# Kernel tuning notes

Measured on AMD Instinct MI355X. Metric: run time of the kernel, lower is better.

The kernel has to match this reference:

```python
import jax, jax.numpy as jnp
import numpy as np
import math

INPUT_SIZE = 2048
OUTPUT_SIZE = 10000
EPS = 1e-8


def _hadamard_cropped(rows, cols):
    # Sylvester Hadamard: H[i, j] = (-1) ** popcount(i & j), built only on the
    i = np.arange(rows, dtype=np.int64)[:, None]
    j = np.arange(cols, dtype=np.int64)[None, :]
    a = i & j
    nbits = max(rows, cols).bit_length()
    parity = np.zeros((rows, cols), dtype=np.int64)
    for k in range(nbits):
        parity += (a >> k) & 1
    return (1 - 2 * (parity & 1)).astype(np.float32)


def setup_inputs() -> dict:
    key = jax.random.key(0)
    kx, kb = jax.random.split(key)
    init_scale = 1.0 / math.sqrt(OUTPUT_SIZE)
    x = jax.random.normal(kx, (16384, INPUT_SIZE), dtype=jnp.float32)
    proj = jnp.asarray(_hadamard_cropped(OUTPUT_SIZE, INPUT_SIZE))
    scale = jnp.full((1,), init_scale, dtype=jnp.float32)
    bias = jax.random.uniform(kb, (OUTPUT_SIZE,), dtype=jnp.float32,
                              minval=-init_scale, maxval=init_scale)
    return {"x": x, "proj": proj, "scale": scale, "bias": bias}


def reference(x, proj, scale, bias):
    # L2-normalize along last dim (norm + eps, matching torch semantics)
    xn = x / (jnp.linalg.norm(x, axis=-1, keepdims=True) + EPS)
    # linear with cropped Hadamard matrix: [B, in] @ [out, in]^T -> [B, out]
    out = -scale * jnp.einsum('bi,oi->bo', xn, proj)
    return out + bias[None, :]
```

## Files before the change

kernel.cpp:

```cpp
#include <hip/hip_runtime.h>
#include <math.h>


typedef float f32x4 __attribute__((ext_vector_type(4)));

constexpr int N_IN  = 2048;
constexpr int N_OUT = 10000;
constexpr int ROWS_PER_BLOCK = 4;

__global__ __launch_bounds__(256, 4) void fwht_proj_kernel(
    const float* __restrict__ x,
    const float* __restrict__ scale,
    const float* __restrict__ bias,
    float* __restrict__ out)
{
    const int wave = threadIdx.x >> 6;
    const int lane = threadIdx.x & 63;
    const int row  = (blockIdx.x << 2) + wave;

    const float* __restrict__ xrow = x + (size_t)row * N_IN;

    f32x4 v[8];
    float ss = 0.0f;
#pragma unroll
    for (int j = 0; j < 8; ++j) {
        v[j] = *reinterpret_cast<const f32x4*>(xrow + (j << 8) + (lane << 2));
        ss = fmaf(v[j].x, v[j].x, ss);
        ss = fmaf(v[j].y, v[j].y, ss);
        ss = fmaf(v[j].z, v[j].z, ss);
        ss = fmaf(v[j].w, v[j].w, ss);
    }
#pragma unroll
    for (int m = 1; m < 64; m <<= 1)
        ss += __shfl_xor(ss, m, 64);
    const float inv = 1.0f / (sqrtf(ss) + 1e-8f);

#pragma unroll
    for (int j = 0; j < 8; ++j) {
        const f32x4 a = v[j];
        f32x4 t;
        t.x = a.x + a.y;  t.y = a.x - a.y;
        t.z = a.z + a.w;  t.w = a.z - a.w;
        f32x4 u;
        u.x = t.x + t.z;  u.y = t.y + t.w;
        u.z = t.x - t.z;  u.w = t.y - t.w;
        v[j] = u;
    }
#pragma unroll
    for (int m = 1; m <= 32; m <<= 1) {
        const bool lo = (lane & m) == 0;
#pragma unroll
        for (int j = 0; j < 8; ++j) {
            f32x4 o;
            o.x = __shfl_xor(v[j].x, m, 64);
            o.y = __shfl_xor(v[j].y, m, 64);
            o.z = __shfl_xor(v[j].z, m, 64);
            o.w = __shfl_xor(v[j].w, m, 64);
            v[j] = lo ? (v[j] + o) : (o - v[j]);
        }
    }
#pragma unroll
    for (int jm = 1; jm <= 4; jm <<= 1) {
#pragma unroll
        for (int j = 0; j < 8; ++j) {
            if ((j & jm) == 0) {
                const f32x4 a = v[j], b = v[j ^ jm];
                v[j]      = a + b;
                v[j ^ jm] = a - b;
            }
        }
    }

    const float s = -scale[0] * inv;
    float* __restrict__ orow = out + (size_t)row * N_OUT;

#pragma unroll
    for (int w = 0; w < 4; ++w) {
#pragma unroll 4
        for (int j = 0; j < 8; ++j) {
            const int o = (w << 11) + (j << 8) + (lane << 2);
            const f32x4 b = *reinterpret_cast<const f32x4*>(bias + o);
            f32x4 r;
            r.x = fmaf(s, v[j].x, b.x);
            r.y = fmaf(s, v[j].y, b.y);
            r.z = fmaf(s, v[j].z, b.z);
            r.w = fmaf(s, v[j].w, b.w);
            *reinterpret_cast<f32x4*>(orow + o) = r;
        }
    }
#pragma unroll 4
    for (int j = 0; j < 7; ++j) {
        const int o = 8192 + (j << 8) + (lane << 2);
        const f32x4 b = *reinterpret_cast<const f32x4*>(bias + o);
        f32x4 r;
        r.x = fmaf(s, v[j].x, b.x);
        r.y = fmaf(s, v[j].y, b.y);
        r.z = fmaf(s, v[j].z, b.z);
        r.w = fmaf(s, v[j].w, b.w);
        *reinterpret_cast<f32x4*>(orow + o) = r;
    }
    if (lane < 4) {
        const int o = 9984 + (lane << 2);
        const f32x4 b = *reinterpret_cast<const f32x4*>(bias + o);
        f32x4 r;
        r.x = fmaf(s, v[7].x, b.x);
        r.y = fmaf(s, v[7].y, b.y);
        r.z = fmaf(s, v[7].z, b.z);
        r.w = fmaf(s, v[7].w, b.w);
        *reinterpret_cast<f32x4*>(orow + o) = r;
    }
}

extern "C" void kernel_launch(void* const* d_in, const int* in_sizes, int n_in,
                              void* d_out, int out_size, void* d_ws, size_t ws_size,
                              hipStream_t stream) {
    const float* x     = (const float*)d_in[0];
    const float* scale = (const float*)d_in[2];
    const float* bias  = (const float*)d_in[3];
    float* out = (float*)d_out;

    const int rows = in_sizes[0] / N_IN;
    dim3 grid(rows / ROWS_PER_BLOCK), block(256);
    hipLaunchKernelGGL(fwht_proj_kernel, grid, block, 0, stream,
                       x, scale, bias, out);
}
```

Measured before the change: 177.4 us.

## Replace cross-lane shuffle butterflies with swizzled LDS transposes in FWHT

Six rounds of 32 shuffle_xor butterflies across lanes are replaced by an in-register butterfly, a transpose through per-wave shared memory with an XOR swizzle, one shuffle stage, and more in-register butterflies. A second swizzled LDS pass puts the results back in output order before the bias-add stores. The aim is to cut the large number of cross-lane shuffle instructions. In exchange it uses 32 KB of LDS per block, which may limit occupancy, and relies on s_waitcnt alone for ordering within each wave.

```diff
diff --git a/kernel.cpp b/kernel.cpp
--- a/kernel.cpp
+++ b/kernel.cpp
@@ -6,7 +6,10 @@
 
 constexpr int N_IN  = 2048;
 constexpr int N_OUT = 10000;
-constexpr int ROWS_PER_BLOCK = 4;
+
+__device__ __forceinline__ int swz(int a) {
+    return a ^ ((((a >> 5) ^ (a >> 8)) & 7) << 2);
+}
 
 __global__ __launch_bounds__(256, 4) void fwht_proj_kernel(
     const float* __restrict__ x,
@@ -14,11 +17,13 @@
     const float* __restrict__ bias,
     float* __restrict__ out)
 {
+    __shared__ float buf[4][N_IN];
+
     const int wave = threadIdx.x >> 6;
     const int lane = threadIdx.x & 63;
-    const int row  = (blockIdx.x << 2) + wave;
-
-    const float* __restrict__ xrow = x + (size_t)row * N_IN;
+    float* __restrict__ my = buf[wave];
+    const size_t row = (size_t)blockIdx.x * 4 + wave;
+    const float* __restrict__ xrow = x + row * N_IN;
 
     f32x4 v[8];
     float ss = 0.0f;
@@ -47,17 +52,51 @@
         v[j] = u;
     }
 #pragma unroll
-    for (int m = 1; m <= 32; m <<= 1) {
-        const bool lo = (lane & m) == 0;
+    for (int jm = 1; jm <= 4; jm <<= 1) {
 #pragma unroll
         for (int j = 0; j < 8; ++j) {
-            f32x4 o;
-            o.x = __shfl_xor(v[j].x, m, 64);
-            o.y = __shfl_xor(v[j].y, m, 64);
-            o.z = __shfl_xor(v[j].z, m, 64);
-            o.w = __shfl_xor(v[j].w, m, 64);
-            v[j] = lo ? (v[j] + o) : (o - v[j]);
+            if ((j & jm) == 0) {
+                const f32x4 a = v[j], b = v[j ^ jm];
+                v[j]      = a + b;
+                v[j ^ jm] = a - b;
+            }
         }
+    }
+
+#pragma unroll
+    for (int j = 0; j < 8; ++j) {
+        my[swz(lane + (j << 7)       )] = v[j].x;
+        my[swz(lane + (j << 7) + 1024)] = v[j].y;
+        my[swz(lane + (j << 7) +   64)] = v[j].z;
+        my[swz(lane + (j << 7) + 1088)] = v[j].w;
+    }
+    asm volatile("s_waitcnt lgkmcnt(0)" ::: "memory");
+#pragma unroll
+    for (int j = 0; j < 8; ++j)
+        v[j] = *reinterpret_cast<const f32x4*>(my + swz((lane << 5) + (j << 2)));
+
+    {
+        const bool lo = (lane & 1) == 0;
+#pragma unroll
+        for (int j = 0; j < 8; ++j) {
+            f32x4 p;
+            p.x = __shfl_xor(v[j].x, 1, 64);
+            p.y = __shfl_xor(v[j].y, 1, 64);
+            p.z = __shfl_xor(v[j].z, 1, 64);
+            p.w = __shfl_xor(v[j].w, 1, 64);
+            v[j] = lo ? (v[j] + p) : (p - v[j]);
+        }
+    }
+#pragma unroll
+    for (int j = 0; j < 8; ++j) {
+        const f32x4 a = v[j];
+        f32x4 t;
+        t.x = a.x + a.y;  t.y = a.x - a.y;
+        t.z = a.z + a.w;  t.w = a.z - a.w;
+        f32x4 u;
+        u.x = t.x + t.z;  u.y = t.y + t.w;
+        u.z = t.x - t.z;  u.w = t.y - t.w;
+        v[j] = u;
     }
 #pragma unroll
     for (int jm = 1; jm <= 4; jm <<= 1) {
@@ -71,42 +110,60 @@
         }
     }
 
+    const int ybase = ((lane & 1) << 7) | (lane & 2) | ((lane & 28) << 6) | ((lane >> 5) & 1);
+#pragma unroll
+    for (int j = 0; j < 8; ++j) {
+        my[swz(ybase + (j << 4)     )] = v[j].x;
+        my[swz(ybase + (j << 4) +  4)] = v[j].y;
+        my[swz(ybase + (j << 4) +  8)] = v[j].z;
+        my[swz(ybase + (j << 4) + 12)] = v[j].w;
+    }
+    asm volatile("s_waitcnt lgkmcnt(0)" ::: "memory");
+
     const float s = -scale[0] * inv;
-    float* __restrict__ orow = out + (size_t)row * N_OUT;
+    float* __restrict__ orow = out + row * N_OUT;
+
+    int yo[8];
+#pragma unroll
+    for (int j = 0; j < 8; ++j)
+        yo[j] = swz((j << 8) + (lane << 2));
 
 #pragma unroll
     for (int w = 0; w < 4; ++w) {
-#pragma unroll 4
+#pragma unroll
         for (int j = 0; j < 8; ++j) {
             const int o = (w << 11) + (j << 8) + (lane << 2);
+            const f32x4 y = *reinterpret_cast<const f32x4*>(my + yo[j]);
             const f32x4 b = *reinterpret_cast<const f32x4*>(bias + o);
             f32x4 r;
-            r.x = fmaf(s, v[j].x, b.x);
-            r.y = fmaf(s, v[j].y, b.y);
-            r.z = fmaf(s, v[j].z, b.z);
-            r.w = fmaf(s, v[j].w, b.w);
+            r.x = fmaf(s, y.x, b.x);
+            r.y = fmaf(s, y.y, b.y);
+            r.z = fmaf(s, y.z, b.z);
+            r.w = fmaf(s, y.w, b.w);
             *reinterpret_cast<f32x4*>(orow + o) = r;
         }
     }
-#pragma unroll 4
+#pragma unroll
     for (int j = 0; j < 7; ++j) {
         const int o = 8192 + (j << 8) + (lane << 2);
+        const f32x4 y = *reinterpret_cast<const f32x4*>(my + yo[j]);
         const f32x4 b = *reinterpret_cast<const f32x4*>(bias + o);
         f32x4 r;
-        r.x = fmaf(s, v[j].x, b.x);
-        r.y = fmaf(s, v[j].y, b.y);
-        r.z = fmaf(s, v[j].z, b.z);
-        r.w = fmaf(s, v[j].w, b.w);
+        r.x = fmaf(s, y.x, b.x);
+        r.y = fmaf(s, y.y, b.y);
+        r.z = fmaf(s, y.z, b.z);
+        r.w = fmaf(s, y.w, b.w);
         *reinterpret_cast<f32x4*>(orow + o) = r;
     }
     if (lane < 4) {
         const int o = 9984 + (lane << 2);
+        const f32x4 y = *reinterpret_cast<const f32x4*>(my + yo[7]);
         const f32x4 b = *reinterpret_cast<const f32x4*>(bias + o);
         f32x4 r;
-        r.x = fmaf(s, v[7].x, b.x);
-        r.y = fmaf(s, v[7].y, b.y);
-        r.z = fmaf(s, v[7].z, b.z);
-        r.w = fmaf(s, v[7].w, b.w);
+        r.x = fmaf(s, y.x, b.x);
+        r.y = fmaf(s, y.y, b.y);
+        r.z = fmaf(s, y.z, b.z);
+        r.w = fmaf(s, y.w, b.w);
         *reinterpret_cast<f32x4*>(orow + o) = r;
     }
 }
@@ -120,7 +177,7 @@
     float* out = (float*)d_out;
 
     const int rows = in_sizes[0] / N_IN;
-    dim3 grid(rows / ROWS_PER_BLOCK), block(256);
+    dim3 grid(rows / 4), block(256);
     hipLaunchKernelGGL(fwht_proj_kernel, grid, block, 0, stream,
                        x, scale, bias, out);
 }
```

Result: faster. 160.2 us, median of 2 (-9.7%).
